# Optimization experiments

Measured on AMD Instinct MI355X. Metric: run time of the kernel, lower is better.

The kernel has to match this reference:

```python
import jax, jax.numpy as jnp
import numpy as np

B, N, D = 4, 2048, 1024
WINDOW = 128

def setup_inputs() -> dict:
    key = jax.random.key(0)
    ks = jax.random.split(key, 5)
    s = 0.02
    return {
        "x": jax.random.normal(ks[0], (B, N, D), dtype=jnp.float32),
        "w_qkv": jax.random.normal(ks[1], (D, 3 * D), dtype=jnp.float32) * s,
        "b_qkv": jax.random.normal(ks[2], (3 * D,), dtype=jnp.float32) * s,
        "w_proj": jax.random.normal(ks[3], (D, D), dtype=jnp.float32) * s,
        "b_proj": jax.random.normal(ks[4], (D,), dtype=jnp.float32) * s,
        "window_size": WINDOW,
    }

def reference(x, w_qkv, b_qkv, w_proj, b_proj, window_size):
    b, n, d = x.shape
    scale = d ** (-0.5)
    qkv = (x @ w_qkv + b_qkv).reshape(b, n, 3, d)
    q, k, v = qkv[:, :, 0], qkv[:, :, 1], qkv[:, :, 2]
    # dense scores with local band mask (faithful to original O(N^2) math)
    attn = jnp.einsum('bnd,bmd->bnm', q, k) * scale
    idx = jnp.arange(n)
    mask_local = jnp.abs(idx[:, None] - idx[None, :]) <= window_size  # [N,N] band
    attn = jnp.where(mask_local[None], attn, -jnp.inf)
    attn = jax.nn.softmax(attn, axis=-1)
    out = jnp.einsum('bnm,bmd->bnd', attn, v)
    return out @ w_proj + b_proj
```

## Files before the change

kernel.cpp:

```cpp
#include <hip/hip_runtime.h>
#include <stdint.h>

typedef __bf16 bf16_t;
typedef __bf16 bf16x8 __attribute__((ext_vector_type(8)));
typedef __bf16 bf16x4 __attribute__((ext_vector_type(4)));
typedef float  f32x4  __attribute__((ext_vector_type(4)));

union U16x8 { uint2 u[2]; bf16x8 v; };

__device__ __forceinline__ void gl_lds16(const void* g, void* l)
{
#if __has_builtin(__builtin_amdgcn_global_load_lds)
    __builtin_amdgcn_global_load_lds(
        (const __attribute__((address_space(1))) unsigned int*)g,
        (__attribute__((address_space(3))) unsigned int*)l, 16, 0, 0);
#else
    *(uint4*)l = *(const uint4*)g;
#endif
}

__global__ void k_convert_bf16(const float* __restrict__ in, bf16_t* __restrict__ out, int n4)
{
    int i = blockIdx.x * blockDim.x + threadIdx.x;
    const int stride = gridDim.x * blockDim.x;
    for (; i < n4; i += stride) {
        float4 v = ((const float4*)in)[i];
        bf16x4 o;
        o[0] = (bf16_t)v.x; o[1] = (bf16_t)v.y; o[2] = (bf16_t)v.z; o[3] = (bf16_t)v.w;
        ((bf16x4*)out)[i] = o;
    }
}

__global__ void k_transpose_bf16(const float* __restrict__ in, bf16_t* __restrict__ out, int R, int C)
{
    __shared__ float tile[32][33];
    const int c0 = blockIdx.x * 32, r0 = blockIdx.y * 32;
    const int tid = threadIdx.x;
    const int c = tid & 31, r = tid >> 5;
#pragma unroll
    for (int i = 0; i < 4; ++i)
        tile[r + i * 8][c] = in[(size_t)(r0 + r + i * 8) * C + (c0 + c)];
    __syncthreads();
#pragma unroll
    for (int i = 0; i < 4; ++i)
        out[(size_t)(c0 + r + i * 8) * R + (r0 + c)] = (bf16_t)tile[c][r + i * 8];
}

template<int MODE>
__global__ __launch_bounds__(256, 2)
void gemm_bt(const bf16_t* __restrict__ A, const bf16_t* __restrict__ Bt,
             const float* __restrict__ bias,
             void* __restrict__ out0, void* __restrict__ out1, void* __restrict__ out2,
             int nbx, int Nn, int K)
{
    __shared__ __align__(16) char smem[34816];
    bf16_t* As = (bf16_t*)smem;
    bf16_t* Bs = (bf16_t*)(smem + 16384);

    const int tid = threadIdx.x;
    const int lane = tid & 63;
    const int w = tid >> 6;
    const int wm = w >> 1, wn = w & 1;
    const int lm = lane & 15, g = lane >> 4;

    const int nwg = gridDim.x;
    const int bid = (blockIdx.x & 7) * (nwg >> 3) + (blockIdx.x >> 3);
    const int bx = bid % nbx, by = bid / nbx;
    const int row0 = by * 128, col0 = bx * 128;

    f32x4 acc[4][4];
#pragma unroll
    for (int i = 0; i < 4; ++i)
#pragma unroll
        for (int j = 0; j < 4; ++j) {
            acc[i][j][0] = 0.f; acc[i][j][1] = 0.f; acc[i][j][2] = 0.f; acc[i][j][3] = 0.f;
        }

    const int nkb = K >> 6;
    for (int kb = 0; kb < nkb; ++kb) {
#pragma unroll
        for (int it = 0; it < 4; ++it) {
            int blk = it * 256 + tid;
            int r = blk >> 3;
            int cb = (blk & 7) << 4;
            int sb = cb ^ ((r & 7) << 4);
            gl_lds16((const char*)(A  + (size_t)(row0 + r) * K + kb * 64) + sb, (char*)As + blk * 16);
            gl_lds16((const char*)(Bt + (size_t)(col0 + r) * K + kb * 64) + sb, (char*)Bs + blk * 16);
        }
        __syncthreads();
#pragma unroll
        for (int kk = 0; kk < 2; ++kk) {
            bf16x8 af[4], bfr[4];
#pragma unroll
            for (int f = 0; f < 4; ++f) {
                int ra = wm * 64 + f * 16 + lm;
                int swa = (ra & 7) << 4;
                int c0b = kk * 64 + g * 8;
                U16x8 u;
                u.u[0] = *(const uint2*)((const char*)As + ra * 128 + (c0b ^ swa));
                u.u[1] = *(const uint2*)((const char*)As + ra * 128 + ((c0b + 32) ^ swa));
                af[f] = u.v;
                int rb = wn * 64 + f * 16 + lm;
                int swb = (rb & 7) << 4;
                U16x8 ub;
                ub.u[0] = *(const uint2*)((const char*)Bs + rb * 128 + (c0b ^ swb));
                ub.u[1] = *(const uint2*)((const char*)Bs + rb * 128 + ((c0b + 32) ^ swb));
                bfr[f] = ub.v;
            }
#pragma unroll
            for (int i = 0; i < 4; ++i)
#pragma unroll
                for (int j = 0; j < 4; ++j)
                    acc[i][j] = __builtin_amdgcn_mfma_f32_16x16x32_bf16(af[i], bfr[j], acc[i][j], 0, 0, 0);
        }
        __syncthreads();
    }

    if constexpr (MODE == 1) {
        float* oo = (float*)out0;
#pragma unroll
        for (int j = 0; j < 4; ++j) {
            int ncol = col0 + wn * 64 + j * 16 + lm;
            float bv = bias[ncol];
#pragma unroll
            for (int i = 0; i < 4; ++i) {
                int rbase = row0 + wm * 64 + i * 16 + g * 4;
#pragma unroll
                for (int r = 0; r < 4; ++r)
                    oo[(size_t)(rbase + r) * Nn + ncol] = acc[i][j][r] + bv;
            }
        }
    } else {
        bf16_t* tile = (bf16_t*)smem;
        constexpr int TP = 136;
        const int region = col0 >> 10;
        if (region < 2) {
#pragma unroll
            for (int j = 0; j < 4; ++j) {
                int cl = wn * 64 + j * 16 + lm;
                float bv = bias[col0 + cl];
#pragma unroll
                for (int i = 0; i < 4; ++i) {
                    int rl = wm * 64 + i * 16 + g * 4;
#pragma unroll
                    for (int r = 0; r < 4; ++r)
                        tile[(rl + r) * TP + cl] = (bf16_t)(acc[i][j][r] + bv);
                }
            }
            __syncthreads();
            bf16_t* dst = (region == 0) ? (bf16_t*)out0 : (bf16_t*)out1;
            const int colbase = col0 & 1023;
#pragma unroll
            for (int it = 0; it < 8; ++it) {
                int blk = it * 256 + tid;
                int rr = blk >> 4;
                int c8 = (blk & 15) * 8;
                uint4 v = *(const uint4*)&tile[rr * TP + c8];
                *(uint4*)(dst + (size_t)(row0 + rr) * 1024 + colbase + c8) = v;
            }
        } else {
#pragma unroll
            for (int j = 0; j < 4; ++j) {
                int cl = wn * 64 + j * 16 + lm;
                float bv = bias[col0 + cl];
#pragma unroll
                for (int i = 0; i < 4; ++i) {
                    int rl = wm * 64 + i * 16 + g * 4;
                    bf16x4 pk;
#pragma unroll
                    for (int r = 0; r < 4; ++r) pk[r] = (bf16_t)(acc[i][j][r] + bv);
                    *(bf16x4*)&tile[cl * TP + rl] = pk;
                }
            }
            __syncthreads();
            bf16_t* vo = (bf16_t*)out2;
            const int bb = row0 >> 11;
            const int n0 = row0 & 2047;
            const int dbase = col0 - 2048;
#pragma unroll
            for (int it = 0; it < 8; ++it) {
                int blk = it * 256 + tid;
                int dl = blk >> 4;
                int n8 = (blk & 15) * 8;
                uint4 v = *(const uint4*)&tile[dl * TP + n8];
                *(uint4*)(vo + (size_t)bb * (1024 * 2048) + (size_t)(dbase + dl) * 2048 + (n0 + n8)) = v;
            }
        }
    }
}

__global__ __launch_bounds__(512, 1)
void k_attn(const bf16_t* __restrict__ Q, const bf16_t* __restrict__ Km,
            const bf16_t* __restrict__ Vt, bf16_t* __restrict__ AO,
            const int* __restrict__ wptr)
{
    constexpr int Nn = 2048, Dd = 1024;
    constexpr int NJT = 18, JROWS = 288;
    __shared__ bf16_t Qs[32][1032];
    __shared__ bf16_t Ks[16][1032];
    __shared__ float  St[JROWS][33];
    __shared__ float  Spart[8][16][36];
    __shared__ float  red[16][32];
    __shared__ float  rowrsum[32];

    const int tid = threadIdx.x;
    const int lane = tid & 63;
    const int w = tid >> 6;
    const int lm = lane & 15, g = lane >> 4;
    const int lblk = (blockIdx.x & 7) * 32 + (blockIdx.x >> 3);
    const int b = lblk >> 6;
    const int q0 = (lblk & 63) * 32;
    const int win = *wptr;
    int jlo = q0 - win; if (jlo < 0) jlo = 0;

    {
        const bf16_t* src = Q + ((size_t)(b * Nn + q0)) * Dd;
#pragma unroll
        for (int i = 0; i < 8; ++i) {
            int c = i * 512 + tid;
            int r = c >> 7;
            int ce = (c & 127) * 8;
            *(uint4*)(&Qs[r][ce]) = *(const uint4*)(src + (size_t)r * Dd + ce);
        }
    }

    for (int jt = 0; jt < NJT; ++jt) {
        __syncthreads();
#pragma unroll
        for (int i = 0; i < 4; ++i) {
            int c = i * 512 + tid;
            int r = c >> 7;
            int ce = (c & 127) * 8;
            int jg = jlo + jt * 16 + r;
            uint4 v = make_uint4(0u, 0u, 0u, 0u);
            if (jg < Nn) v = *(const uint4*)(Km + ((size_t)(b * Nn + jg)) * Dd + ce);
            *(uint4*)(&Ks[r][ce]) = v;
        }
        __syncthreads();
        f32x4 sacc[2];
#pragma unroll
        for (int f = 0; f < 2; ++f) { sacc[f][0]=0.f; sacc[f][1]=0.f; sacc[f][2]=0.f; sacc[f][3]=0.f; }
#pragma unroll
        for (int ks = 0; ks < 4; ++ks) {
            int d0 = w * 128 + ks * 32;
            U16x8 kf;
            kf.u[0] = *(const uint2*)(&Ks[lm][d0 + g * 4]);
            kf.u[1] = *(const uint2*)(&Ks[lm][d0 + 16 + g * 4]);
#pragma unroll
            for (int f = 0; f < 2; ++f) {
                U16x8 qf;
                qf.u[0] = *(const uint2*)(&Qs[f * 16 + lm][d0 + g * 4]);
                qf.u[1] = *(const uint2*)(&Qs[f * 16 + lm][d0 + 16 + g * 4]);
                sacc[f] = __builtin_amdgcn_mfma_f32_16x16x32_bf16(qf.v, kf.v, sacc[f], 0, 0, 0);
            }
        }
#pragma unroll
        for (int f = 0; f < 2; ++f)
            *(f32x4*)(&Spart[w][lm][f * 16 + g * 4]) = sacc[f];
        __syncthreads();
        {
            int j = tid >> 5;
            int qq = tid & 31;
            float s = 0.f;
#pragma unroll
            for (int s2 = 0; s2 < 8; ++s2) s += Spart[s2][j][qq];
            s *= 0.03125f;
            int jg = jlo + jt * 16 + j;
            int qg = q0 + qq;
            int dd = qg - jg; if (dd < 0) dd = -dd;
            bool valid = (jg < Nn) && (dd <= win);
            St[jt * 16 + j][qq] = valid ? s : -3.0e38f;
        }
    }
    __syncthreads();

    {
        int qq = tid & 31, sub = tid >> 5;
        float m = -3.0e38f;
        for (int j = sub; j < JROWS; j += 16) m = fmaxf(m, St[j][qq]);
        red[sub][qq] = m;
        __syncthreads();
        float mm = red[0][qq];
#pragma unroll
        for (int s2 = 1; s2 < 16; ++s2) mm = fmaxf(mm, red[s2][qq]);
        __syncthreads();
        float sum = 0.f;
        for (int j = sub; j < JROWS; j += 16) {
            float p = __expf(St[j][qq] - mm);
            St[j][qq] = p;
            sum += p;
        }
        red[sub][qq] = sum;
        __syncthreads();
        float ss = 0.f;
#pragma unroll
        for (int s2 = 0; s2 < 16; ++s2) ss += red[s2][qq];
        if (sub == 0) rowrsum[qq] = 1.f / ss;
    }
    __syncthreads();

    f32x4 oacc[2][8];
#pragma unroll
    for (int f = 0; f < 2; ++f)
#pragma unroll
        for (int nf = 0; nf < 8; ++nf) { oacc[f][nf][0]=0.f; oacc[f][nf][1]=0.f; oacc[f][nf][2]=0.f; oacc[f][nf][3]=0.f; }

    const bf16_t* vbase = Vt + (size_t)b * Dd * Nn;
#pragma unroll 1
    for (int ks = 0; ks < 9; ++ks) {
        int jb = ks * 32;
        bf16x8 pf[2];
#pragma unroll
        for (int f = 0; f < 2; ++f) {
            int qq = f * 16 + lm;
            bf16x8 v;
#pragma unroll
            for (int h = 0; h < 2; ++h)
#pragma unroll
                for (int i2 = 0; i2 < 4; ++i2)
                    v[h * 4 + i2] = (bf16_t)St[jb + h * 16 + g * 4 + i2][qq];
            pf[f] = v;
        }
        U16x8 bl[8];
        int j0g = jlo + jb + g * 4;      if (j0g > Nn - 4) j0g = Nn - 4;
        int j1g = jlo + jb + 16 + g * 4; if (j1g > Nn - 4) j1g = Nn - 4;
#pragma unroll
        for (int nf = 0; nf < 8; ++nf) {
            int d = w * 128 + nf * 16 + lm;
            const bf16_t* vp = vbase + (size_t)d * Nn;
            bl[nf].u[0] = *(const uint2*)(vp + j0g);
            bl[nf].u[1] = *(const uint2*)(vp + j1g);
        }
#pragma unroll
        for (int nf = 0; nf < 8; ++nf)
#pragma unroll
            for (int f = 0; f < 2; ++f)
                oacc[f][nf] = __builtin_amdgcn_mfma_f32_16x16x32_bf16(pf[f], bl[nf].v, oacc[f][nf], 0, 0, 0);
    }

#pragma unroll
    for (int f = 0; f < 2; ++f) {
#pragma unroll
        for (int r = 0; r < 4; ++r) {
            int qq = f * 16 + g * 4 + r;
            float rs = rowrsum[qq];
            size_t rowg = (size_t)(b * Nn + q0 + qq) * Dd;
#pragma unroll
            for (int nf = 0; nf < 8; ++nf) {
                int d = w * 128 + nf * 16 + lm;
                AO[rowg + d] = (bf16_t)(oacc[f][nf][r] * rs);
            }
        }
    }
}

extern "C" void kernel_launch(void* const* d_in, const int* in_sizes, int n_in,
                              void* d_out, int out_size, void* d_ws, size_t ws_size,
                              hipStream_t stream)
{
    (void)in_sizes; (void)n_in; (void)out_size; (void)ws_size;
    const float* x      = (const float*)d_in[0];
    const float* w_qkv  = (const float*)d_in[1];
    const float* b_qkv  = (const float*)d_in[2];
    const float* w_proj = (const float*)d_in[3];
    const float* b_proj = (const float*)d_in[4];
    const int*   wsz    = (const int*)d_in[5];
    float* out = (float*)d_out;

    constexpr int Bb = 4, Nn = 2048, Dd = 1024;
    constexpr int M = Bb * Nn, N3 = 3 * Dd;

    char* p = (char*)d_ws;
    bf16_t* xb     = (bf16_t*)p; p += (size_t)M * Dd * 2;
    bf16_t* wqkvT  = (bf16_t*)p; p += (size_t)N3 * Dd * 2;
    bf16_t* wprojT = (bf16_t*)p; p += (size_t)Dd * Dd * 2;
    bf16_t* qb     = (bf16_t*)p; p += (size_t)M * Dd * 2;
    bf16_t* kb     = (bf16_t*)p; p += (size_t)M * Dd * 2;
    bf16_t* vtb    = (bf16_t*)p; p += (size_t)M * Dd * 2;
    bf16_t* ao     = xb;

    k_convert_bf16<<<2048, 256, 0, stream>>>(x, xb, M * Dd / 4);
    k_transpose_bf16<<<dim3(N3 / 32, Dd / 32), 256, 0, stream>>>(w_qkv, wqkvT, Dd, N3);
    k_transpose_bf16<<<dim3(Dd / 32, Dd / 32), 256, 0, stream>>>(w_proj, wprojT, Dd, Dd);
    gemm_bt<0><<<1536, 256, 0, stream>>>(xb, wqkvT, b_qkv, qb, kb, vtb, 24, N3, Dd);
    k_attn<<<Bb * (Nn / 32), 512, 0, stream>>>(qb, kb, vtb, ao, wsz);
    gemm_bt<1><<<512, 256, 0, stream>>>(ao, wprojT, b_proj, out, nullptr, nullptr, 8, Dd, Dd);
}
```

Measured before the change: 272.3 us.

## Split QK^T score tiles across waves instead of splitting the head dimension

The score computation now gives each wave whole 16-key tiles over the full 1024-wide dimension, reading K directly from global memory into registers. Previously all waves split the dimension and reduced partial sums through shared memory, with three barriers per tile. This removes the K staging buffer, the cross-wave partial reduction and most barriers. The costs are uncoalesced-ish direct global K loads and imbalance, since 18 tiles over 8 waves leaves some waves with three tiles. The unroll-1 pragma on the PV loop is also dropped.

```diff
diff --git a/kernel.cpp b/kernel.cpp
--- a/kernel.cpp
+++ b/kernel.cpp
@@ -6,7 +6,7 @@
 typedef __bf16 bf16x4 __attribute__((ext_vector_type(4)));
 typedef float  f32x4  __attribute__((ext_vector_type(4)));
 
-union U16x8 { uint2 u[2]; bf16x8 v; };
+union U16x8 { uint2 u[2]; uint4 q; bf16x8 v; };
 
 __device__ __forceinline__ void gl_lds16(const void* g, void* l)
 {
@@ -197,9 +197,7 @@
     constexpr int Nn = 2048, Dd = 1024;
     constexpr int NJT = 18, JROWS = 288;
     __shared__ bf16_t Qs[32][1032];
-    __shared__ bf16_t Ks[16][1032];
-    __shared__ float  St[JROWS][33];
-    __shared__ float  Spart[8][16][36];
+    __shared__ float  St[JROWS][36];
     __shared__ float  red[16][32];
     __shared__ float  rowrsum[32];
 
@@ -223,53 +221,34 @@
             *(uint4*)(&Qs[r][ce]) = *(const uint4*)(src + (size_t)r * Dd + ce);
         }
     }
-
-    for (int jt = 0; jt < NJT; ++jt) {
-        __syncthreads();
-#pragma unroll
-        for (int i = 0; i < 4; ++i) {
-            int c = i * 512 + tid;
-            int r = c >> 7;
-            int ce = (c & 127) * 8;
-            int jg = jlo + jt * 16 + r;
-            uint4 v = make_uint4(0u, 0u, 0u, 0u);
-            if (jg < Nn) v = *(const uint4*)(Km + ((size_t)(b * Nn + jg)) * Dd + ce);
-            *(uint4*)(&Ks[r][ce]) = v;
-        }
-        __syncthreads();
+    __syncthreads();
+
+    for (int t = w; t < NJT; t += 8) {
+        const int j16 = jlo + t * 16;
+        int krow = j16 + lm; if (krow > Nn - 1) krow = Nn - 1;
+        const bf16_t* kp = Km + ((size_t)(b * Nn + krow)) * Dd + g * 8;
         f32x4 sacc[2];
 #pragma unroll
         for (int f = 0; f < 2; ++f) { sacc[f][0]=0.f; sacc[f][1]=0.f; sacc[f][2]=0.f; sacc[f][3]=0.f; }
-#pragma unroll
-        for (int ks = 0; ks < 4; ++ks) {
-            int d0 = w * 128 + ks * 32;
-            U16x8 kf;
-            kf.u[0] = *(const uint2*)(&Ks[lm][d0 + g * 4]);
-            kf.u[1] = *(const uint2*)(&Ks[lm][d0 + 16 + g * 4]);
-#pragma unroll
-            for (int f = 0; f < 2; ++f) {
-                U16x8 qf;
-                qf.u[0] = *(const uint2*)(&Qs[f * 16 + lm][d0 + g * 4]);
-                qf.u[1] = *(const uint2*)(&Qs[f * 16 + lm][d0 + 16 + g * 4]);
-                sacc[f] = __builtin_amdgcn_mfma_f32_16x16x32_bf16(qf.v, kf.v, sacc[f], 0, 0, 0);
-            }
-        }
-#pragma unroll
-        for (int f = 0; f < 2; ++f)
-            *(f32x4*)(&Spart[w][lm][f * 16 + g * 4]) = sacc[f];
-        __syncthreads();
-        {
-            int j = tid >> 5;
-            int qq = tid & 31;
-            float s = 0.f;
-#pragma unroll
-            for (int s2 = 0; s2 < 8; ++s2) s += Spart[s2][j][qq];
-            s *= 0.03125f;
-            int jg = jlo + jt * 16 + j;
-            int qg = q0 + qq;
-            int dd = qg - jg; if (dd < 0) dd = -dd;
-            bool valid = (jg < Nn) && (dd <= win);
-            St[jt * 16 + j][qq] = valid ? s : -3.0e38f;
+#pragma unroll 4
+        for (int kc = 0; kc < 32; ++kc) {
+            U16x8 kf, q0f, q1f;
+            kf.q  = *(const uint4*)(kp + kc * 32);
+            q0f.q = *(const uint4*)(&Qs[lm][kc * 32 + g * 8]);
+            q1f.q = *(const uint4*)(&Qs[16 + lm][kc * 32 + g * 8]);
+            sacc[0] = __builtin_amdgcn_mfma_f32_16x16x32_bf16(kf.v, q0f.v, sacc[0], 0, 0, 0);
+            sacc[1] = __builtin_amdgcn_mfma_f32_16x16x32_bf16(kf.v, q1f.v, sacc[1], 0, 0, 0);
+        }
+#pragma unroll
+        for (int f = 0; f < 2; ++f) {
+            int qg = q0 + f * 16 + lm;
+#pragma unroll
+            for (int r = 0; r < 4; ++r) {
+                int jg = j16 + g * 4 + r;
+                int dd2 = qg - jg; if (dd2 < 0) dd2 = -dd2;
+                bool valid = (jg < Nn) && (dd2 <= win);
+                St[t * 16 + g * 4 + r][f * 16 + lm] = valid ? sacc[f][r] * 0.03125f : -3.0e38f;
+            }
         }
     }
     __syncthreads();
@@ -306,7 +285,6 @@
         for (int nf = 0; nf < 8; ++nf) { oacc[f][nf][0]=0.f; oacc[f][nf][1]=0.f; oacc[f][nf][2]=0.f; oacc[f][nf][3]=0.f; }
 
     const bf16_t* vbase = Vt + (size_t)b * Dd * Nn;
-#pragma unroll 1
     for (int ks = 0; ks < 9; ++ks) {
         int jb = ks * 32;
         bf16x8 pf[2];
```

New measurement: 253.4 us. -6.9%, faster.
